# Kernel tuning notes

Hardware: AMD Instinct MI355X
Metric: run time of the kernel (lower is better)

Reference implementation:

```python
import jax, jax.numpy as jnp
import numpy as np
import math

LOG2PI = math.log(2 * math.pi)
K = 16           # num_comp
C = 64           # channels
S, NN, T = 2, 207, 12
NFEAT = S * NN * T  # 4968 = in_features of the Conv1d(k=1) projections


def setup_inputs() -> dict:
    key = jax.random.key(0)
    ks = jax.random.split(key, 7)
    x = jax.random.normal(ks[0], (8, C, S, NN, T), dtype=jnp.float32)
    scale = 0.02
    alpha_w = jax.random.normal(ks[1], (K, NFEAT), dtype=jnp.float32) * scale
    alpha_b = jax.random.normal(ks[2], (K,), dtype=jnp.float32) * scale
    sigma_w = jax.random.normal(ks[3], (K, NFEAT), dtype=jnp.float32) * scale
    sigma_b = jax.random.normal(ks[4], (K,), dtype=jnp.float32) * scale
    mu_w = jax.random.normal(ks[5], (K, NFEAT), dtype=jnp.float32) * scale
    mu_b = jax.random.normal(ks[6], (K,), dtype=jnp.float32) * scale
    return {"x": x, "alpha_w": alpha_w, "alpha_b": alpha_b,
            "sigma_w": sigma_w, "sigma_b": sigma_b, "mu_w": mu_w, "mu_b": mu_b}


def reference(x, alpha_w, alpha_b, sigma_w, sigma_b, mu_w, mu_b):
    b, c, s, n, t = x.shape
    hd = x.reshape(b, c, -1)                       # (b, c, N); torch's hd after final permute
    # Conv1d(kernel=1) over the (b, N, c) layout == per-(b,c) linear N -> K
    def proj(w, bias):
        return jnp.einsum('bcn,kn->bck', hd, w) + bias  # (b, c, K)
    alphas = jax.nn.softmax(proj(alpha_w, alpha_b), axis=-1)   # softmax over K
    sigma = jnp.exp(proj(sigma_w, sigma_b))                    # (b, c, K)
    mu = proj(mu_w, mu_b)                                      # (b, c, K)

    # log N(h | mu_k, sigma_k^2): (b, c, N, K) via broadcasting (original repeats)
    z = (hd[..., None] - mu[:, :, None, :]) / sigma[:, :, None, :]
    log_component_prob = -jnp.log(sigma)[:, :, None, :] - 0.5 * LOG2PI - 0.5 * z * z
    log_prob = log_component_prob + jnp.log(alphas)[:, :, None, :]
    # original computes log(sum(exp(.))) without max-subtraction; replicate exactly
    log_sum = jnp.log(jnp.sum(jnp.exp(log_prob), axis=-1, keepdims=True))
    weightedlogPdf = log_prob - log_sum                        # (b, c, N, K)
    labels = jnp.argmax(weightedlogPdf, axis=-1)               # (b, c, N) int

    # cluster_norm: due to torch aliasing (new_mu = new_sigma = labels, same storage),
    # both end up equal to sigma gathered by label, so norm uses sigma_g for center+scale.
    sigma_g = jnp.take_along_axis(sigma, labels, axis=2)       # (b, c, N)
    norm = (hd - sigma_g) / (sigma_g + 1e-5)
    out = norm.reshape(b, c, s, n, t)

    # probability regularization loss
    first_item = jnp.mean(jnp.exp(weightedlogPdf) * log_component_prob)
    q_z = jnp.mean(weightedlogPdf, axis=2)                     # (b, c, K)
    kl = jnp.mean(alphas * (jnp.log(alphas) - q_z))            # F.kl_div(q_z, alphas, 'mean')
    loss = kl - first_item
    return out, loss
```

## Files before the change

kernel.cpp:

```cpp
#include <hip/hip_runtime.h>
#include <math.h>

#define NROWS 512
#define NFEAT 4968
#define NVEC4 1242
#define KSLICES 6
#define SLICE4 207
#define GSL 1242
#define HALF_LOG2PI 0.91893853320467274178032973640562

__global__ __launch_bounds__(256) void proj_kernel(
    const float* __restrict__ x,
    const float* __restrict__ aw,
    const float* __restrict__ sw,
    const float* __restrict__ mw,
    double* __restrict__ pp)
{
    const int rowtile = blockIdx.x & 63;
    const int jg      = (blockIdx.x >> 6) % 3;
    const int sl      = blockIdx.x / 192;
    const int t = threadIdx.x;
    const int j = t >> 4;
    const int s16 = t & 15;
    const int row0 = rowtile * 8;

    const float* W = (jg == 0) ? aw : (jg == 1) ? sw : mw;
    const float4* wp = (const float4*)(W + (size_t)j * NFEAT) + sl * SLICE4;
    const float4* xp = (const float4*)(x + (size_t)row0 * NFEAT) + sl * SLICE4;

    double acc[8][2];
    #pragma unroll
    for (int r = 0; r < 8; ++r) { acc[r][0] = 0.0; acc[r][1] = 0.0; }

    for (int i = s16; i < SLICE4; i += 16) {
        float4 wv = wp[i];
        #pragma unroll
        for (int r = 0; r < 8; ++r) {
            float4 xv = xp[(size_t)r * NVEC4 + i];
            acc[r][0] = fma((double)xv.x, (double)wv.x, acc[r][0]);
            acc[r][0] = fma((double)xv.y, (double)wv.y, acc[r][0]);
            acc[r][1] = fma((double)xv.z, (double)wv.z, acc[r][1]);
            acc[r][1] = fma((double)xv.w, (double)wv.w, acc[r][1]);
        }
    }

    #pragma unroll
    for (int r = 0; r < 8; ++r) {
        double a = acc[r][0] + acc[r][1];
        #pragma unroll
        for (int off = 8; off; off >>= 1) a += __shfl_xor(a, off, 16);
        if (s16 == 0)
            pp[((size_t)(row0 + r) * 48 + jg * 16 + j) * KSLICES + sl] = a;
    }
}

__global__ __launch_bounds__(256) void params_kernel(
    const double* __restrict__ pp,
    const float* __restrict__ ab,
    const float* __restrict__ sb,
    const float* __restrict__ mb,
    double* __restrict__ mu, double* __restrict__ isg, double* __restrict__ cl,
    double* __restrict__ sig, double* __restrict__ ivp,
    float* __restrict__ la, float* __restrict__ al)
{
    const int g = blockIdx.x * 256 + threadIdx.x;
    const int row = g >> 4, k = g & 15;
    const double* p = pp + ((size_t)row * 48 + k) * KSLICES;

    double pa = 0.0, ps = 0.0, pm = 0.0;
    #pragma unroll
    for (int s = 0; s < KSLICES; ++s) {
        pa += p[s];
        ps += p[16 * KSLICES + s];
        pm += p[32 * KSLICES + s];
    }
    pa += (double)ab[k]; ps += (double)sb[k]; pm += (double)mb[k];

    double m = pa;
    #pragma unroll
    for (int off = 8; off; off >>= 1) m = fmax(m, __shfl_xor(m, off, 16));
    double e = exp(pa - m);
    double ss = e;
    #pragma unroll
    for (int off = 8; off; off >>= 1) ss += __shfl_xor(ss, off, 16);
    double alpha = e / ss;
    double lav = log(alpha);

    double sg  = exp(ps);
    double lsg = log(sg);

    mu[g]  = pm;
    isg[g] = 1.0 / sg;
    cl[g]  = lav - lsg - HALF_LOG2PI;
    sig[g] = sg;
    ivp[g] = 1.0 / (sg + 1e-5);
    la[g]  = (float)lav;
    al[g]  = (float)alpha;
}

__global__ __launch_bounds__(256) void gmm_kernel(
    const float* __restrict__ x,
    const double* __restrict__ mu, const double* __restrict__ isg,
    const double* __restrict__ cl, const float* __restrict__ laf,
    const double* __restrict__ sig, const double* __restrict__ ivp,
    float* __restrict__ out,
    float* __restrict__ S1p, float* __restrict__ S2p, float* __restrict__ FIp)
{
    const int row = blockIdx.x >> 2;
    const int sl  = blockIdx.x & 3;
    const int tid = threadIdx.x;
    const int g0  = row * 16;

    __shared__ double sig_s[16], ivp_s[16];
    __shared__ float  red[4][18];
    __shared__ float  tot_s[18];

    if (tid < 16) {
        sig_s[tid] = sig[g0 + tid];
        ivp_s[tid] = ivp[g0 + tid];
    }
    __syncthreads();

    double mu_r[16], isg_r[16], cl_r[16];
    float  la_r[16];
    #pragma unroll
    for (int k = 0; k < 16; ++k) {
        mu_r[k]  = mu[g0 + k];
        isg_r[k] = isg[g0 + k];
        cl_r[k]  = cl[g0 + k];
        la_r[k]  = laf[g0 + k];
    }

    float S1[16];
    #pragma unroll
    for (int k = 0; k < 16; ++k) S1[k] = 0.f;
    float S2 = 0.f, FI = 0.f;

    const float* xr = x + (size_t)row * NFEAT + sl * GSL;
    float* outr = out + (size_t)row * NFEAT + sl * GSL;

    for (int n = tid; n < GSL; n += 256) {
        double h = (double)xr[n];
        double maxlp = -1.0e300;
        int lab = 0;
        float sumexp = 0.f, s1 = 0.f;
        #pragma unroll
        for (int k = 0; k < 16; ++k) {
            double z  = (h - mu_r[k]) * isg_r[k];
            double lp = fma(z * z, -0.5, cl_r[k]);
            if (lp > maxlp) { maxlp = lp; lab = k; }
            float lpf = (float)lp;
            float e   = __expf(lpf);
            float lcp = lpf - la_r[k];
            sumexp += e;
            s1 = fmaf(e, lcp, s1);
            S1[k] += lcp;
        }
        S2 += __logf(sumexp);
        FI += s1 / sumexp;

        double sg = sig_s[lab];
        outr[n] = (float)((h - sg) * ivp_s[lab]);
    }

    float vals[18];
    #pragma unroll
    for (int i = 0; i < 16; ++i) vals[i] = S1[i];
    vals[16] = S2; vals[17] = FI;

    #pragma unroll
    for (int i = 0; i < 18; ++i) {
        float v = vals[i];
        #pragma unroll
        for (int off = 32; off; off >>= 1) v += __shfl_xor(v, off, 64);
        vals[i] = v;
    }
    const int wave = tid >> 6, lane = tid & 63;
    if (lane == 0) {
        #pragma unroll
        for (int i = 0; i < 18; ++i) red[wave][i] = vals[i];
    }
    __syncthreads();
    if (tid < 18)
        tot_s[tid] = red[0][tid] + red[1][tid] + red[2][tid] + red[3][tid];
    __syncthreads();
    if (tid < 16) S1p[(size_t)blockIdx.x * 16 + tid] = tot_s[tid];
    if (tid == 16) S2p[blockIdx.x] = tot_s[16];
    if (tid == 17) FIp[blockIdx.x] = tot_s[17];
}

__global__ __launch_bounds__(1024) void loss_kernel(
    const float* __restrict__ S1p, const float* __restrict__ S2p,
    const float* __restrict__ FIp,
    const float* __restrict__ la, const float* __restrict__ al,
    float* __restrict__ loss_out)
{
    const int tid = threadIdx.x;
    const float invN = 1.0f / (float)NFEAT;

    float kl_acc = 0.f;
    for (int g = tid; g < 8192; g += 1024) {
        int row = g >> 4, k = g & 15;
        int b = row * 4;
        float s1 = S1p[(size_t)(b + 0) * 16 + k] + S1p[(size_t)(b + 1) * 16 + k]
                 + S1p[(size_t)(b + 2) * 16 + k] + S1p[(size_t)(b + 3) * 16 + k];
        float s2 = S2p[b + 0] + S2p[b + 1] + S2p[b + 2] + S2p[b + 3];
        float lav = la[g], alv = al[g];
        float q = s1 * invN + lav - s2 * invN;
        kl_acc += alv * (lav - q);
    }
    float fi_acc = 0.f;
    for (int i = tid; i < 2048; i += 1024) fi_acc += FIp[i];

    #pragma unroll
    for (int off = 32; off; off >>= 1) {
        kl_acc += __shfl_xor(kl_acc, off, 64);
        fi_acc += __shfl_xor(fi_acc, off, 64);
    }
    __shared__ float ra[16], rb[16];
    const int wave = tid >> 6, lane = tid & 63;
    if (lane == 0) { ra[wave] = kl_acc; rb[wave] = fi_acc; }
    __syncthreads();
    if (tid == 0) {
        float ka = 0.f, kb = 0.f;
        #pragma unroll
        for (int i = 0; i < 16; ++i) { ka += ra[i]; kb += rb[i]; }
        loss_out[0] = ka / 8192.0f - kb / 40697856.0f;
    }
}

extern "C" void kernel_launch(void* const* d_in, const int* in_sizes, int n_in,
                              void* d_out, int out_size, void* d_ws, size_t ws_size,
                              hipStream_t stream) {
    const float* x  = (const float*)d_in[0];
    const float* aw = (const float*)d_in[1];
    const float* ab = (const float*)d_in[2];
    const float* sw = (const float*)d_in[3];
    const float* sb = (const float*)d_in[4];
    const float* mw = (const float*)d_in[5];
    const float* mb = (const float*)d_in[6];
    float* out = (float*)d_out;

    double* pp  = (double*)d_ws;
    double* mu  = pp + (size_t)NROWS * 48 * KSLICES;
    double* isg = mu + 8192;
    double* cl  = isg + 8192;
    double* sig = cl + 8192;
    double* ivp = sig + 8192;
    float* la   = (float*)(ivp + 8192);
    float* al   = la + 8192;
    float* S1p  = al + 8192;
    float* S2p  = S1p + 2048 * 16;
    float* FIp  = S2p + 2048;

    proj_kernel<<<64 * 3 * KSLICES, 256, 0, stream>>>(x, aw, sw, mw, pp);
    params_kernel<<<32, 256, 0, stream>>>(pp, ab, sb, mb, mu, isg, cl, sig, ivp, la, al);
    gmm_kernel<<<NROWS * 4, 256, 0, stream>>>(x, mu, isg, cl, la, sig, ivp,
                                              out, S1p, S2p, FIp);
    loss_kernel<<<1, 1024, 0, stream>>>(S1p, S2p, FIp, la, al,
                                        out + (size_t)NROWS * NFEAT);
}
```

Before: 58.18 us.

## Use fp32 GMM inner loop with fp64 fallback for near-tie argmax

The per-element mixture loop now evaluates the 16 component log-probabilities in fp32 instead of fp64, tracking the top two values. When the best and second-best are within a small margin, it recomputes the argmax in fp64 so the labels match the double-precision reference. The projection kernel also halves its rows per block (4 instead of 8), doubling the grid to spread the fp64 dot products across more workgroups. The cost is extra fp32 parameter arrays and a divergent fallback path.

Result: slower. 82.11 us (+41.1%).

```diff
diff --git a/kernel.cpp b/kernel.cpp
--- a/kernel.cpp
+++ b/kernel.cpp
@@ -16,26 +16,26 @@
     const float* __restrict__ mw,
     double* __restrict__ pp)
 {
-    const int rowtile = blockIdx.x & 63;
-    const int jg      = (blockIdx.x >> 6) % 3;
-    const int sl      = blockIdx.x / 192;
+    const int rt = blockIdx.x & 127;
+    const int jg = (blockIdx.x >> 7) % 3;
+    const int sl = blockIdx.x / 384;
     const int t = threadIdx.x;
     const int j = t >> 4;
     const int s16 = t & 15;
-    const int row0 = rowtile * 8;
+    const int row0 = rt * 4;
 
     const float* W = (jg == 0) ? aw : (jg == 1) ? sw : mw;
     const float4* wp = (const float4*)(W + (size_t)j * NFEAT) + sl * SLICE4;
     const float4* xp = (const float4*)(x + (size_t)row0 * NFEAT) + sl * SLICE4;
 
-    double acc[8][2];
-    #pragma unroll
-    for (int r = 0; r < 8; ++r) { acc[r][0] = 0.0; acc[r][1] = 0.0; }
+    double acc[4][2];
+    #pragma unroll
+    for (int r = 0; r < 4; ++r) { acc[r][0] = 0.0; acc[r][1] = 0.0; }
 
     for (int i = s16; i < SLICE4; i += 16) {
         float4 wv = wp[i];
         #pragma unroll
-        for (int r = 0; r < 8; ++r) {
+        for (int r = 0; r < 4; ++r) {
             float4 xv = xp[(size_t)r * NVEC4 + i];
             acc[r][0] = fma((double)xv.x, (double)wv.x, acc[r][0]);
             acc[r][0] = fma((double)xv.y, (double)wv.y, acc[r][0]);
@@ -45,7 +45,7 @@
     }
 
     #pragma unroll
-    for (int r = 0; r < 8; ++r) {
+    for (int r = 0; r < 4; ++r) {
         double a = acc[r][0] + acc[r][1];
         #pragma unroll
         for (int off = 8; off; off >>= 1) a += __shfl_xor(a, off, 16);
@@ -61,6 +61,7 @@
     const float* __restrict__ mb,
     double* __restrict__ mu, double* __restrict__ isg, double* __restrict__ cl,
     double* __restrict__ sig, double* __restrict__ ivp,
+    float* __restrict__ muf, float* __restrict__ isgf, float* __restrict__ clf,
     float* __restrict__ la, float* __restrict__ al)
 {
     const int g = blockIdx.x * 256 + threadIdx.x;
@@ -89,11 +90,17 @@
     double sg  = exp(ps);
     double lsg = log(sg);
 
+    double isgv = 1.0 / sg;
+    double clv  = lav - lsg - HALF_LOG2PI;
+
     mu[g]  = pm;
-    isg[g] = 1.0 / sg;
-    cl[g]  = lav - lsg - HALF_LOG2PI;
+    isg[g] = isgv;
+    cl[g]  = clv;
     sig[g] = sg;
     ivp[g] = 1.0 / (sg + 1e-5);
+    muf[g]  = (float)pm;
+    isgf[g] = (float)isgv;
+    clf[g]  = (float)clv;
     la[g]  = (float)lav;
     al[g]  = (float)alpha;
 }
@@ -101,7 +108,9 @@
 __global__ __launch_bounds__(256) void gmm_kernel(
     const float* __restrict__ x,
     const double* __restrict__ mu, const double* __restrict__ isg,
-    const double* __restrict__ cl, const float* __restrict__ laf,
+    const double* __restrict__ cl,
+    const float* __restrict__ muf, const float* __restrict__ isgf,
+    const float* __restrict__ clf, const float* __restrict__ laf,
     const double* __restrict__ sig, const double* __restrict__ ivp,
     float* __restrict__ out,
     float* __restrict__ S1p, float* __restrict__ S2p, float* __restrict__ FIp)
@@ -121,13 +130,12 @@
     }
     __syncthreads();
 
-    double mu_r[16], isg_r[16], cl_r[16];
-    float  la_r[16];
+    float mu_r[16], isg_r[16], cl_r[16], la_r[16];
     #pragma unroll
     for (int k = 0; k < 16; ++k) {
-        mu_r[k]  = mu[g0 + k];
-        isg_r[k] = isg[g0 + k];
-        cl_r[k]  = cl[g0 + k];
+        mu_r[k]  = muf[g0 + k];
+        isg_r[k] = isgf[g0 + k];
+        cl_r[k]  = clf[g0 + k];
         la_r[k]  = laf[g0 + k];
     }
 
@@ -140,27 +148,38 @@
     float* outr = out + (size_t)row * NFEAT + sl * GSL;
 
     for (int n = tid; n < GSL; n += 256) {
-        double h = (double)xr[n];
-        double maxlp = -1.0e300;
+        float h = xr[n];
+        float max1 = -3.4e38f, max2 = -3.4e38f;
         int lab = 0;
         float sumexp = 0.f, s1 = 0.f;
         #pragma unroll
         for (int k = 0; k < 16; ++k) {
-            double z  = (h - mu_r[k]) * isg_r[k];
-            double lp = fma(z * z, -0.5, cl_r[k]);
-            if (lp > maxlp) { maxlp = lp; lab = k; }
-            float lpf = (float)lp;
-            float e   = __expf(lpf);
-            float lcp = lpf - la_r[k];
+            float z  = (h - mu_r[k]) * isg_r[k];
+            float lp = fmaf(z * z, -0.5f, cl_r[k]);
+            if (lp > max1) { max2 = max1; max1 = lp; lab = k; }
+            else if (lp > max2) { max2 = lp; }
+            float e   = __expf(lp);
+            float lcp = lp - la_r[k];
             sumexp += e;
             s1 = fmaf(e, lcp, s1);
             S1[k] += lcp;
         }
+        if (max1 - max2 < 1e-3f) {
+            double hd = (double)h;
+            double maxlp = -1.0e300;
+            lab = 0;
+            #pragma unroll
+            for (int k = 0; k < 16; ++k) {
+                double zd  = (hd - mu[g0 + k]) * isg[g0 + k];
+                double lpd = fma(zd * zd, -0.5, cl[g0 + k]);
+                if (lpd > maxlp) { maxlp = lpd; lab = k; }
+            }
+        }
         S2 += __logf(sumexp);
         FI += s1 / sumexp;
 
         double sg = sig_s[lab];
-        outr[n] = (float)((h - sg) * ivp_s[lab]);
+        outr[n] = (float)(((double)h - sg) * ivp_s[lab]);
     }
 
     float vals[18];
@@ -247,15 +266,21 @@
     double* cl  = isg + 8192;
     double* sig = cl + 8192;
     double* ivp = sig + 8192;
-    float* la   = (float*)(ivp + 8192);
+    float* muf  = (float*)(ivp + 8192);
+    float* isgf = muf + 8192;
+    float* clf  = isgf + 8192;
+    float* la   = clf + 8192;
     float* al   = la + 8192;
     float* S1p  = al + 8192;
     float* S2p  = S1p + 2048 * 16;
     float* FIp  = S2p + 2048;
 
-    proj_kernel<<<64 * 3 * KSLICES, 256, 0, stream>>>(x, aw, sw, mw, pp);
-    params_kernel<<<32, 256, 0, stream>>>(pp, ab, sb, mb, mu, isg, cl, sig, ivp, la, al);
-    gmm_kernel<<<NROWS * 4, 256, 0, stream>>>(x, mu, isg, cl, la, sig, ivp,
+    proj_kernel<<<128 * 3 * KSLICES, 256, 0, stream>>>(x, aw, sw, mw, pp);
+    params_kernel<<<32, 256, 0, stream>>>(pp, ab, sb, mb,
+                                          mu, isg, cl, sig, ivp,
+                                          muf, isgf, clf, la, al);
+    gmm_kernel<<<NROWS * 4, 256, 0, stream>>>(x, mu, isg, cl,
+                                              muf, isgf, clf, la, sig, ivp,
                                               out, S1p, S2p, FIp);
     loss_kernel<<<1, 1024, 0, stream>>>(S1p, S2p, FIp, la, al,
                                         out + (size_t)NROWS * NFEAT);
```
